# Optimization experiments

Measured on AMD Instinct MI355X. Metric: run time of the kernel, lower is better.

Reference implementation:

```python
import jax, jax.numpy as jnp
import numpy as np

IN_F, OUT_F = 4096, 4096
GROUP = 128
N_GROUPS = IN_F // GROUP
R, NUM_A, NUM_B = 16, 2, 2
LORA_ALPHA = 32
SCALING = LORA_ALPHA / R  # 2.0
BITS = 4
PACK = 32 // BITS  # 8 int4 per int32


def dequant_gptq(qweight, qzeros, scales, g_idx):
    """Unpack int4 GPTQ weights -> dense [in_features, out_features] fp32."""
    shifts = (jnp.arange(PACK, dtype=jnp.int32) * BITS)
    # qweight: [in/8, out] packed along in dim
    wq = (qweight[:, None, :] >> shifts[None, :, None]) & 0xF       # [in/8, 8, out]
    wq = wq.reshape(IN_F, OUT_F).astype(jnp.float32)
    # qzeros: [n_groups, out/8] packed along out dim
    zq = (qzeros[:, :, None] >> shifts[None, None, :]) & 0xF        # [g, out/8, 8]
    zq = zq.reshape(N_GROUPS, OUT_F).astype(jnp.float32)
    # per-row group lookup
    return scales[g_idx] * (wq - zq[g_idx])                          # [in, out]


def activation_weights(x, normalize=True):
    # 'inps' mode: per-input-feature importance from mean |activation|
    w = jnp.mean(jnp.abs(x), axis=tuple(range(x.ndim - 1)))          # [in]
    if normalize:
        w = w / (jnp.mean(w) + 1e-6)
    return w


def setup_inputs() -> dict:
    key = jax.random.key(0)
    ks = jax.random.split(key, 8)
    x = jax.random.normal(ks[0], (2, 2048, IN_F), dtype=jnp.float32)
    scales = jax.random.uniform(ks[1], (N_GROUPS, OUT_F), dtype=jnp.float32) * 0.01 + 0.001
    bias = jax.random.normal(ks[2], (OUT_F,), dtype=jnp.float32) * 0.01
    lora_A = jax.random.normal(ks[3], (NUM_A, R, IN_F), dtype=jnp.float32) * (1.0 / np.sqrt(IN_F))
    lora_B = jax.random.normal(ks[4], (NUM_B, OUT_F, R), dtype=jnp.float32) * 0.01
    qweight = jax.random.randint(ks[5], (IN_F // PACK, OUT_F), 0, 2147483647, dtype=jnp.int32)
    qzeros = jax.random.randint(ks[6], (N_GROUPS, OUT_F // PACK), 0, 2147483647, dtype=jnp.int32)
    g_idx = (jnp.arange(IN_F, dtype=jnp.int32) // GROUP).astype(jnp.int32)
    return {"x": x, "scales": scales, "bias": bias, "lora_A": lora_A,
            "lora_B": lora_B, "qweight": qweight, "qzeros": qzeros, "g_idx": g_idx}


def reference(x, scales, bias, lora_A, lora_B, qweight, qzeros, g_idx):
    W = dequant_gptq(qweight, qzeros, scales, g_idx)                 # [in, out]
    result = jnp.einsum('bsi,io->bso', x, W) + bias                  # base GPTQ linear
    # activation-aware 'inps' weighting (dropout p=0 -> identity, eval mode)
    aw = activation_weights(x, normalize=True)                       # [in]
    x_w = x * aw                                                     # broadcast on last dim
    # sum_{i,j} B_j(A_i(x_w)) == (sum_j B_j) @ (sum_i A_i) @ x_w (all linear, no bias)
    A_sum = jnp.sum(lora_A, axis=0)                                  # [r, in]
    B_sum = jnp.sum(lora_B, axis=0)                                  # [out, r]
    h = jnp.einsum('bsi,ri->bsr', x_w, A_sum)                        # [b, s, r]
    result = result + jnp.einsum('bsr,or->bso', h, B_sum) * SCALING
    return result
```

## Files before the change

kernel.cpp:

```cpp
#include <hip/hip_runtime.h>
#include <stdint.h>

#define IN_F 4096
#define OUT_F 4096

typedef __attribute__((ext_vector_type(4))) float f32x4;
typedef _Float16 f16x8 __attribute__((ext_vector_type(8)));
typedef _Float16 f16x2 __attribute__((ext_vector_type(2)));
typedef unsigned short u16x8 __attribute__((ext_vector_type(8)));

__device__ __forceinline__ unsigned short f2h(float f) {
  _Float16 h = (_Float16)f;
  return __builtin_bit_cast(unsigned short, h);
}

#define SIGMA_TAB 0x73625140u

#define OFF_XH     ((size_t)0)
#define OFF_PART   ((size_t)33554432)
#define OFF_W      ((size_t)35651584)
#define OFF_BSUM   ((size_t)35667968)
#define OFF_AW     ((size_t)35668480)
#define OFF_BS     ((size_t)35799552)
#define OFF_HPART  ((size_t)36061696)
#define OFF_HB     ((size_t)38158848)
#define WS_NEED    ((size_t)38420992)

__global__ __launch_bounds__(256) void k1_prep(const float* __restrict__ x,
                                               unsigned short* __restrict__ xh,
                                               float* __restrict__ part) {
  int t = threadIdx.x;
  int c8 = (blockIdx.x * 256 + t) * 8;
  int by = blockIdx.y;
  float a[8];
  #pragma unroll
  for (int i = 0; i < 8; ++i) a[i] = 0.f;
  for (int rr = 0; rr < 32; ++rr) {
    size_t off = (size_t)(by * 32 + rr) * IN_F + c8;
    f32x4 v0 = *(const f32x4*)(x + off);
    f32x4 v1 = *(const f32x4*)(x + off + 4);
    u16x8 o;
    o[0] = f2h(v0[0]); o[1] = f2h(v1[0]); o[2] = f2h(v0[1]); o[3] = f2h(v1[1]);
    o[4] = f2h(v0[2]); o[5] = f2h(v1[2]); o[6] = f2h(v0[3]); o[7] = f2h(v1[3]);
    *(u16x8*)(xh + off) = o;
    a[0] += fabsf(v0[0]); a[1] += fabsf(v0[1]); a[2] += fabsf(v0[2]); a[3] += fabsf(v0[3]);
    a[4] += fabsf(v1[0]); a[5] += fabsf(v1[1]); a[6] += fabsf(v1[2]); a[7] += fabsf(v1[3]);
  }
  f32x4 p0 = { a[0], a[1], a[2], a[3] };
  f32x4 p1 = { a[4], a[5], a[6], a[7] };
  *(f32x4*)(part + (size_t)by * IN_F + c8) = p0;
  *(f32x4*)(part + (size_t)by * IN_F + c8 + 4) = p1;
}

__global__ __launch_bounds__(256) void k2_colred(const float* __restrict__ part,
                                                 float* __restrict__ w,
                                                 float* __restrict__ bsum) {
  int t = threadIdx.x;
  int col = blockIdx.x * 256 + t;
  float s = 0.f;
  for (int st = 0; st < 128; ++st) s += part[(size_t)st * IN_F + col];
  float wv = s * (1.0f / 4096.0f);
  w[col] = wv;
  __shared__ float red[256];
  red[t] = wv; __syncthreads();
  for (int k = 128; k > 0; k >>= 1) { if (t < k) red[t] += red[t + k]; __syncthreads(); }
  if (t == 0) bsum[blockIdx.x] = red[0];
}

__global__ __launch_bounds__(256) void k3_fold(const float* __restrict__ lora_A,
                                               const float* __restrict__ lora_B,
                                               const float* __restrict__ w,
                                               const float* __restrict__ bsum,
                                               unsigned short* __restrict__ A_w,
                                               unsigned short* __restrict__ Bs) {
  int b = blockIdx.x, t = threadIdx.x;
  float s = 0.f;
  #pragma unroll
  for (int i = 0; i < 16; ++i) s += bsum[i];
  float iv = 1.0f / (s * (1.0f / 4096.0f) + 1e-6f);
  if (b < 256) {
    int idx = b * 256 + t;
    int r = idx >> 12;
    int pos = idx & 4095;
    int p = pos & 7;
    int orig = (pos & ~7) + (int)((SIGMA_TAB >> (p * 4)) & 7);
    float v = (lora_A[(size_t)r * IN_F + orig] + lora_A[(size_t)(16 + r) * IN_F + orig]) * w[orig] * iv;
    A_w[idx] = f2h(v);
  } else {
    int idx = (b - 256) * 256 + t;
    int o = idx >> 5, r = idx & 31;
    float v = 0.f;
    if (r < 16) v = 2.0f * (lora_B[o * 16 + r] + lora_B[OUT_F * 16 + o * 16 + r]);
    Bs[idx] = f2h(v);
  }
}

__global__ __launch_bounds__(256) void k4_h(const unsigned short* __restrict__ xh,
                                            const unsigned short* __restrict__ A_w,
                                            float* __restrict__ hpart) {
  int mb = blockIdx.x, kc = blockIdx.y;
  int t = threadIdx.x, wid = t >> 6, l = t & 63;
  int m0 = mb * 128 + wid * 32;
  int lr = l & 15, lg = l >> 4;
  f32x4 z = { 0.f, 0.f, 0.f, 0.f };
  f32x4 acc0 = z, acc1 = z;
  for (int it = 0; it < 16; ++it) {
    int k = kc * 512 + it * 32 + lg * 8;
    f16x8 b  = *(const f16x8*)(A_w + (size_t)lr * IN_F + k);
    f16x8 a0 = *(const f16x8*)(xh + (size_t)(m0 + lr) * IN_F + k);
    f16x8 a1 = *(const f16x8*)(xh + (size_t)(m0 + 16 + lr) * IN_F + k);
    acc0 = __builtin_amdgcn_mfma_f32_16x16x32_f16(a0, b, acc0, 0, 0, 0);
    acc1 = __builtin_amdgcn_mfma_f32_16x16x32_f16(a1, b, acc1, 0, 0, 0);
  }
  float* hp = hpart + (size_t)kc * IN_F * 16;
  #pragma unroll
  for (int r = 0; r < 4; ++r) {
    hp[(size_t)(m0 + lg * 4 + r) * 16 + lr]      = acc0[r];
    hp[(size_t)(m0 + 16 + lg * 4 + r) * 16 + lr] = acc1[r];
  }
}

__global__ __launch_bounds__(256) void k5_hred(const float* __restrict__ hpart,
                                               unsigned short* __restrict__ hb) {
  int gid = blockIdx.x * 256 + threadIdx.x;
  int m = gid >> 5, r = gid & 31;
  float v = 0.f;
  if (r < 16)
    for (int kc = 0; kc < 8; ++kc) v += hpart[(size_t)kc * 65536 + m * 16 + r];
  hb[gid] = f2h(v);
}

__device__ __forceinline__ f16x8 deq8(unsigned int q, f16x2 s2, f16x2 zz2) {
  unsigned int u0 = ( q         & 0x000F000Fu) | 0x64006400u;
  unsigned int u1 = ((q >> 4)   & 0x000F000Fu) | 0x64006400u;
  unsigned int u2 = ((q >> 8)   & 0x000F000Fu) | 0x64006400u;
  unsigned int u3 = ((q >> 12)  & 0x000F000Fu) | 0x64006400u;
  f16x2 w0 = (__builtin_bit_cast(f16x2, u0) - zz2) * s2;
  f16x2 w1 = (__builtin_bit_cast(f16x2, u1) - zz2) * s2;
  f16x2 w2 = (__builtin_bit_cast(f16x2, u2) - zz2) * s2;
  f16x2 w3 = (__builtin_bit_cast(f16x2, u3) - zz2) * s2;
  struct { f16x2 a, b, c, d; } r { w0, w1, w2, w3 };
  return __builtin_bit_cast(f16x8, r);
}

__global__ __launch_bounds__(256) void k6_gemm(const unsigned short* __restrict__ xh,
                                               const int* __restrict__ qweight,
                                               const int* __restrict__ qzeros,
                                               const float* __restrict__ scales,
                                               const float* __restrict__ bias,
                                               const unsigned short* __restrict__ hb,
                                               const unsigned short* __restrict__ Bs,
                                               float* __restrict__ out) {
  __shared__ __align__(16) unsigned short As[2][128 * 64];
  int t = threadIdx.x, w = t >> 6, l = t & 63;
  int lr = l & 15, lg = l >> 4;
  int b0 = blockIdx.x;
  int bid = (b0 & 7) * 128 + (b0 >> 3);
  int mt = bid >> 5, nt = bid & 31;
  int m0 = mt * 128, n0 = nt * 128;
  int ncol0 = n0 + w * 32 + lr;

  f32x4 zz = { 0.f, 0.f, 0.f, 0.f };
  f32x4 acc[8][2];
  #pragma unroll
  for (int m = 0; m < 8; ++m) { acc[m][0] = zz; acc[m][1] = zz; }

  #define STAGE_A(BUF, KT) do {                                                   \
    int k0_ = (KT) * 64;                                                          \
    _Pragma("unroll")                                                             \
    for (int it = 0; it < 4; ++it) {                                              \
      int idx = it * 256 + t;                                                     \
      int row = idx >> 3, c = idx & 7;                                            \
      int cp = c ^ (row & 7);                                                     \
      const unsigned short* gp = xh + (size_t)(m0 + row) * IN_F + k0_ + cp * 8;   \
      __builtin_amdgcn_global_load_lds((const __attribute__((address_space(1))) void*)gp, \
                                       (__attribute__((address_space(3))) void*)(&As[BUF][0] + idx * 8), \
                                       16, 0, 0);                                 \
    }                                                                             \
  } while (0)

  #define LOAD_QW(QW, KT) do {                                                    \
    int k0_ = (KT) * 64;                                                          \
    _Pragma("unroll")                                                             \
    for (int ks = 0; ks < 2; ++ks)                                                \
      _Pragma("unroll")                                                           \
      for (int j = 0; j < 2; ++j)                                                 \
        QW[j][ks] = (unsigned int)qweight[(size_t)((k0_ >> 3) + ks * 4 + lg) * OUT_F + ncol0 + j * 16]; \
  } while (0)

  #define LOAD_CONST(S2, ZP, GRP) do {                                            \
    _Pragma("unroll")                                                             \
    for (int j = 0; j < 2; ++j) {                                                 \
      int n = ncol0 + j * 16;                                                     \
      float s_ = scales[(size_t)(GRP) * OUT_F + n];                               \
      unsigned int zi = (unsigned int)qzeros[(GRP) * (OUT_F / 8) + (n >> 3)];     \
      unsigned int z = (zi >> ((n & 7) * 4)) & 0xFu;                              \
      unsigned int zzu = 0x64006400u + z * 0x00010001u;                           \
      ZP[j] = __builtin_bit_cast(f16x2, zzu);                                     \
      _Float16 sh = (_Float16)s_;                                                 \
      unsigned int sb = (unsigned int)__builtin_bit_cast(unsigned short, sh);     \
      unsigned int ssu = (sb << 16) | sb;                                         \
      S2[j] = __builtin_bit_cast(f16x2, ssu);                                     \
    }                                                                             \
  } while (0)

  #define COMPUTE(BUF, QW) do {                                                   \
    f16x8 bf[2][2];                                                               \
    _Pragma("unroll")                                                             \
    for (int ks = 0; ks < 2; ++ks)                                                \
      _Pragma("unroll")                                                           \
      for (int j = 0; j < 2; ++j)                                                 \
        bf[j][ks] = deq8(QW[j][ks], s2c[j], zpc[j]);                              \
    _Pragma("unroll")                                                             \
    for (int ks = 0; ks < 2; ++ks) {                                              \
      f16x8 a[8];                                                                 \
      _Pragma("unroll")                                                           \
      for (int m = 0; m < 8; ++m) {                                               \
        int row = m * 16 + lr;                                                    \
        int chunk = (ks * 4 + lg) ^ (lr & 7);                                     \
        a[m] = *(const f16x8*)(&As[BUF][0] + row * 64 + chunk * 8);               \
      }                                                                           \
      __builtin_amdgcn_s_setprio(1);                                              \
      _Pragma("unroll")                                                           \
      for (int m = 0; m < 8; ++m) {                                               \
        acc[m][0] = __builtin_amdgcn_mfma_f32_16x16x32_f16(a[m], bf[0][ks], acc[m][0], 0, 0, 0); \
        acc[m][1] = __builtin_amdgcn_mfma_f32_16x16x32_f16(a[m], bf[1][ks], acc[m][1], 0, 0, 0); \
      }                                                                           \
      __builtin_amdgcn_s_setprio(0);                                              \
    }                                                                             \
  } while (0)

  unsigned int qwA[2][2], qwB[2][2];
  f16x2 s2c[2], zpc[2];

  STAGE_A(0, 0);
  LOAD_QW(qwA, 0);
  LOAD_CONST(s2c, zpc, 0);
  __syncthreads();

  for (int kt = 0; kt < 64; kt += 2) {
    STAGE_A(1, kt + 1);
    LOAD_QW(qwB, kt + 1);
    COMPUTE(0, qwA);
    __syncthreads();
    bool more = (kt + 2 < 64);
    f16x2 s2n[2], zpn[2];
    if (more) {
      STAGE_A(0, kt + 2);
      LOAD_QW(qwA, kt + 2);
      LOAD_CONST(s2n, zpn, (kt + 2) >> 1);
    }
    COMPUTE(1, qwB);
    __syncthreads();
    if (more) {
      s2c[0] = s2n[0]; s2c[1] = s2n[1];
      zpc[0] = zpn[0]; zpc[1] = zpn[1];
    }
  }
  #undef STAGE_A
  #undef LOAD_QW
  #undef LOAD_CONST
  #undef COMPUTE

  {
    f16x8 bb[2];
    #pragma unroll
    for (int j = 0; j < 2; ++j)
      bb[j] = *(const f16x8*)(Bs + (size_t)(ncol0 + j * 16) * 32 + lg * 8);
    #pragma unroll
    for (int m = 0; m < 8; ++m) {
      f16x8 ah = *(const f16x8*)(hb + (size_t)(m0 + m * 16 + lr) * 32 + lg * 8);
      acc[m][0] = __builtin_amdgcn_mfma_f32_16x16x32_f16(ah, bb[0], acc[m][0], 0, 0, 0);
      acc[m][1] = __builtin_amdgcn_mfma_f32_16x16x32_f16(ah, bb[1], acc[m][1], 0, 0, 0);
    }
  }
  #pragma unroll
  for (int j = 0; j < 2; ++j) {
    int ocol = ncol0 + j * 16;
    float bv = bias[ocol];
    #pragma unroll
    for (int m = 0; m < 8; ++m) {
      int orow = m0 + m * 16 + lg * 4;
      #pragma unroll
      for (int r = 0; r < 4; ++r)
        out[(size_t)(orow + r) * OUT_F + ocol] = acc[m][j][r] + bv;
    }
  }
}

extern "C" void kernel_launch(void* const* d_in, const int* in_sizes, int n_in,
                              void* d_out, int out_size, void* d_ws, size_t ws_size,
                              hipStream_t stream) {
  const float* x       = (const float*)d_in[0];
  const float* scales  = (const float*)d_in[1];
  const float* bias    = (const float*)d_in[2];
  const float* lora_A  = (const float*)d_in[3];
  const float* lora_B  = (const float*)d_in[4];
  const int*   qweight = (const int*)d_in[5];
  const int*   qzeros  = (const int*)d_in[6];
  float* out = (float*)d_out;

  if (ws_size < WS_NEED) return;

  char* ws = (char*)d_ws;
  unsigned short* xh  = (unsigned short*)(ws + OFF_XH);
  float* part         = (float*)(ws + OFF_PART);
  float* w            = (float*)(ws + OFF_W);
  float* bsum         = (float*)(ws + OFF_BSUM);
  unsigned short* A_w = (unsigned short*)(ws + OFF_AW);
  unsigned short* Bs  = (unsigned short*)(ws + OFF_BS);
  float* hpart        = (float*)(ws + OFF_HPART);
  unsigned short* hb  = (unsigned short*)(ws + OFF_HB);

  k1_prep<<<dim3(2, 128), 256, 0, stream>>>(x, xh, part);
  k2_colred<<<16, 256, 0, stream>>>(part, w, bsum);
  k3_fold<<<768, 256, 0, stream>>>(lora_A, lora_B, w, bsum, A_w, Bs);
  k4_h<<<dim3(32, 8), 256, 0, stream>>>(xh, A_w, hpart);
  k5_hred<<<512, 256, 0, stream>>>(hpart, hb);
  k6_gemm<<<1024, 256, 0, stream>>>(xh, qweight, qzeros, scales, bias, hb, Bs, out);
}
```

Before: 191.4 us.

## Enlarge GEMM block tile to 256x256 with eight waves of 128x64

The fused dequant GEMM moves from 128x128 tiles with 4 waves to 256x256 tiles with 8 waves, each wave computing 128x64. Each thread dequantizes twice as many columns and issues 4 MFMAs per A fragment, which improves reuse of both the shared-memory A tile and the dequantized weights and halves redundant global traffic for x and qweight. The cost is double the LDS (64KB), more accumulator registers (128 floats), and only 256 blocks on a large-CU device, which risks lower occupancy and a worse tail.

```diff
diff --git a/kernel.cpp b/kernel.cpp
--- a/kernel.cpp
+++ b/kernel.cpp
@@ -143,33 +143,36 @@
   return __builtin_bit_cast(f16x8, r);
 }
 
-__global__ __launch_bounds__(256) void k6_gemm(const unsigned short* __restrict__ xh,
-                                               const int* __restrict__ qweight,
-                                               const int* __restrict__ qzeros,
-                                               const float* __restrict__ scales,
-                                               const float* __restrict__ bias,
-                                               const unsigned short* __restrict__ hb,
-                                               const unsigned short* __restrict__ Bs,
-                                               float* __restrict__ out) {
-  __shared__ __align__(16) unsigned short As[2][128 * 64];
-  int t = threadIdx.x, w = t >> 6, l = t & 63;
+__global__ __launch_bounds__(512, 2) void k6_gemm(const unsigned short* __restrict__ xh,
+                                                  const int* __restrict__ qweight,
+                                                  const int* __restrict__ qzeros,
+                                                  const float* __restrict__ scales,
+                                                  const float* __restrict__ bias,
+                                                  const unsigned short* __restrict__ hb,
+                                                  const unsigned short* __restrict__ Bs,
+                                                  float* __restrict__ out) {
+  __shared__ __align__(16) unsigned short As[2][256 * 64];
+  int t = threadIdx.x, wid = t >> 6, l = t & 63;
   int lr = l & 15, lg = l >> 4;
   int b0 = blockIdx.x;
-  int bid = (b0 & 7) * 128 + (b0 >> 3);
-  int mt = bid >> 5, nt = bid & 31;
-  int m0 = mt * 128, n0 = nt * 128;
-  int ncol0 = n0 + w * 32 + lr;
+  int bid = (b0 & 7) * 32 + (b0 >> 3);
+  int mt = bid >> 4, nt = bid & 15;
+  int m0 = mt * 256, n0 = nt * 256;
+  int wm = wid >> 2, wn = wid & 3;
+  int ncol0 = n0 + wn * 64 + lr;
 
   f32x4 zz = { 0.f, 0.f, 0.f, 0.f };
-  f32x4 acc[8][2];
-  #pragma unroll
-  for (int m = 0; m < 8; ++m) { acc[m][0] = zz; acc[m][1] = zz; }
+  f32x4 acc[8][4];
+  #pragma unroll
+  for (int m = 0; m < 8; ++m)
+    #pragma unroll
+    for (int j = 0; j < 4; ++j) acc[m][j] = zz;
 
   #define STAGE_A(BUF, KT) do {                                                   \
     int k0_ = (KT) * 64;                                                          \
     _Pragma("unroll")                                                             \
     for (int it = 0; it < 4; ++it) {                                              \
-      int idx = it * 256 + t;                                                     \
+      int idx = it * 512 + t;                                                     \
       int row = idx >> 3, c = idx & 7;                                            \
       int cp = c ^ (row & 7);                                                     \
       const unsigned short* gp = xh + (size_t)(m0 + row) * IN_F + k0_ + cp * 8;   \
@@ -184,13 +187,13 @@
     _Pragma("unroll")                                                             \
     for (int ks = 0; ks < 2; ++ks)                                                \
       _Pragma("unroll")                                                           \
-      for (int j = 0; j < 2; ++j)                                                 \
+      for (int j = 0; j < 4; ++j)                                                 \
         QW[j][ks] = (unsigned int)qweight[(size_t)((k0_ >> 3) + ks * 4 + lg) * OUT_F + ncol0 + j * 16]; \
   } while (0)
 
   #define LOAD_CONST(S2, ZP, GRP) do {                                            \
     _Pragma("unroll")                                                             \
-    for (int j = 0; j < 2; ++j) {                                                 \
+    for (int j = 0; j < 4; ++j) {                                                 \
       int n = ncol0 + j * 16;                                                     \
       float s_ = scales[(size_t)(GRP) * OUT_F + n];                               \
       unsigned int zi = (unsigned int)qzeros[(GRP) * (OUT_F / 8) + (n >> 3)];     \
@@ -205,33 +208,31 @@
   } while (0)
 
   #define COMPUTE(BUF, QW) do {                                                   \
-    f16x8 bf[2][2];                                                               \
-    _Pragma("unroll")                                                             \
-    for (int ks = 0; ks < 2; ++ks)                                                \
-      _Pragma("unroll")                                                           \
-      for (int j = 0; j < 2; ++j)                                                 \
-        bf[j][ks] = deq8(QW[j][ks], s2c[j], zpc[j]);                              \
     _Pragma("unroll")                                                             \
     for (int ks = 0; ks < 2; ++ks) {                                              \
+      f16x8 bf[4];                                                                \
+      _Pragma("unroll")                                                           \
+      for (int j = 0; j < 4; ++j)                                                 \
+        bf[j] = deq8(QW[j][ks], s2c[j], zpc[j]);                                  \
       f16x8 a[8];                                                                 \
       _Pragma("unroll")                                                           \
       for (int m = 0; m < 8; ++m) {                                               \
-        int row = m * 16 + lr;                                                    \
+        int row = wm * 128 + m * 16 + lr;                                         \
         int chunk = (ks * 4 + lg) ^ (lr & 7);                                     \
         a[m] = *(const f16x8*)(&As[BUF][0] + row * 64 + chunk * 8);               \
       }                                                                           \
       __builtin_amdgcn_s_setprio(1);                                              \
       _Pragma("unroll")                                                           \
-      for (int m = 0; m < 8; ++m) {                                               \
-        acc[m][0] = __builtin_amdgcn_mfma_f32_16x16x32_f16(a[m], bf[0][ks], acc[m][0], 0, 0, 0); \
-        acc[m][1] = __builtin_amdgcn_mfma_f32_16x16x32_f16(a[m], bf[1][ks], acc[m][1], 0, 0, 0); \
-      }                                                                           \
+      for (int m = 0; m < 8; ++m)                                                 \
+        _Pragma("unroll")                                                         \
+        for (int j = 0; j < 4; ++j)                                               \
+          acc[m][j] = __builtin_amdgcn_mfma_f32_16x16x32_f16(a[m], bf[j], acc[m][j], 0, 0, 0); \
       __builtin_amdgcn_s_setprio(0);                                              \
     }                                                                             \
   } while (0)
 
-  unsigned int qwA[2][2], qwB[2][2];
-  f16x2 s2c[2], zpc[2];
+  unsigned int qwA[4][2], qwB[4][2];
+  f16x2 s2c[4], zpc[4];
 
   STAGE_A(0, 0);
   LOAD_QW(qwA, 0);
@@ -244,7 +245,7 @@
     COMPUTE(0, qwA);
     __syncthreads();
     bool more = (kt + 2 < 64);
-    f16x2 s2n[2], zpn[2];
+    f16x2 s2n[4], zpn[4];
     if (more) {
       STAGE_A(0, kt + 2);
       LOAD_QW(qwA, kt + 2);
@@ -253,8 +254,8 @@
     COMPUTE(1, qwB);
     __syncthreads();
     if (more) {
-      s2c[0] = s2n[0]; s2c[1] = s2n[1];
-      zpc[0] = zpn[0]; zpc[1] = zpn[1];
+      #pragma unroll
+      for (int j = 0; j < 4; ++j) { s2c[j] = s2n[j]; zpc[j] = zpn[j]; }
     }
   }
   #undef STAGE_A
@@ -263,24 +264,25 @@
   #undef COMPUTE
 
   {
-    f16x8 bb[2];
+    f16x8 bb[4];
     #pragma unroll
-    for (int j = 0; j < 2; ++j)
+    for (int j = 0; j < 4; ++j)
       bb[j] = *(const f16x8*)(Bs + (size_t)(ncol0 + j * 16) * 32 + lg * 8);
     #pragma unroll
     for (int m = 0; m < 8; ++m) {
-      f16x8 ah = *(const f16x8*)(hb + (size_t)(m0 + m * 16 + lr) * 32 + lg * 8);
-      acc[m][0] = __builtin_amdgcn_mfma_f32_16x16x32_f16(ah, bb[0], acc[m][0], 0, 0, 0);
-      acc[m][1] = __builtin_amdgcn_mfma_f32_16x16x32_f16(ah, bb[1], acc[m][1], 0, 0, 0);
+      f16x8 ah = *(const f16x8*)(hb + (size_t)(m0 + wm * 128 + m * 16 + lr) * 32 + lg * 8);
+      #pragma unroll
+      for (int j = 0; j < 4; ++j)
+        acc[m][j] = __builtin_amdgcn_mfma_f32_16x16x32_f16(ah, bb[j], acc[m][j], 0, 0, 0);
     }
   }
   #pragma unroll
-  for (int j = 0; j < 2; ++j) {
+  for (int j = 0; j < 4; ++j) {
     int ocol = ncol0 + j * 16;
     float bv = bias[ocol];
     #pragma unroll
     for (int m = 0; m < 8; ++m) {
-      int orow = m0 + m * 16 + lg * 4;
+      int orow = m0 + wm * 128 + m * 16 + lg * 4;
       #pragma unroll
       for (int r = 0; r < 4; ++r)
         out[(size_t)(orow + r) * OUT_F + ocol] = acc[m][j][r] + bv;
@@ -317,5 +319,5 @@
   k3_fold<<<768, 256, 0, stream>>>(lora_A, lora_B, w, bsum, A_w, Bs);
   k4_h<<<dim3(32, 8), 256, 0, stream>>>(xh, A_w, hpart);
   k5_hred<<<512, 256, 0, stream>>>(hpart, hb);
-  k6_gemm<<<1024, 256, 0, stream>>>(xh, qweight, qzeros, scales, bias, hb, Bs, out);
-}
+  k6_gemm<<<256, 512, 0, stream>>>(xh, qweight, qzeros, scales, bias, hb, Bs, out);
+}
```

After: 263.6 us. 1.38x slower.
